# Performance work log

Measured on AMD Instinct MI355X. Metric: run time of the kernel, lower is better.

Reference implementation:

```python
import jax, jax.numpy as jnp
import numpy as np

EMBED_DIM = 512
NUM_HEADS = 8
HEAD_DIM = EMBED_DIM // NUM_HEADS
SEQ = 1024
BSZ = 8
T1 = 0.6
T2 = 0.4
MAX_NEG = -jnp.finfo(jnp.float32).max


def setup_inputs() -> dict:
    key = jax.random.key(0)
    ks = jax.random.split(key, 10)
    shp = (SEQ, BSZ, EMBED_DIM)
    inv = 1.0 / np.sqrt(EMBED_DIM)
    return {
        "query": jax.random.normal(ks[0], shp, jnp.float32),
        "key": jax.random.normal(ks[1], shp, jnp.float32),
        "value": jax.random.normal(ks[2], shp, jnp.float32),
        "query_sem": jax.random.normal(ks[3], shp, jnp.float32),
        "key_sem": jax.random.normal(ks[4], shp, jnp.float32),
        "sem_map": jax.random.uniform(ks[5], (SEQ, SEQ), jnp.float32),
        "in_proj_weight": jax.random.normal(ks[6], (3 * EMBED_DIM, EMBED_DIM), jnp.float32) * inv,
        "in_proj_bias": jnp.zeros((3 * EMBED_DIM,), jnp.float32),
        "out_proj_weight": jax.random.normal(ks[7], (EMBED_DIM, EMBED_DIM), jnp.float32) * inv,
        "out_proj_bias": jnp.zeros((EMBED_DIM,), jnp.float32),
    }


def _heads(x):
    # [T, B, E] -> [B*H, T, head_dim]
    T, B, E = x.shape
    return jnp.transpose(x.reshape(T, B * NUM_HEADS, HEAD_DIM), (1, 0, 2))


def _attn_path(qx, kx, vx, sem_map, Wi, bi, Wo, bo, ssa):
    # packed in-projection (generic path: q, k, v are distinct tensors)
    Wq, Wk, Wv = jnp.split(Wi, 3, axis=0)
    bq, bk, bv = jnp.split(bi, 3)
    q = _heads(qx @ Wq.T + bq)
    k = _heads(kx @ Wk.T + bk)
    v = _heads(vx @ Wv.T + bv)
    scale = 1.0 / np.sqrt(HEAD_DIM)
    scores = jnp.einsum("bte,bse->bts", q * scale, k)  # [B*H, T, S]
    scores = jnp.where(sem_map[None, :, :] < 0.5, MAX_NEG, scores)
    if ssa:
        # keep only the argmax entry per row, others set to max_neg
        idx = jnp.argmax(scores, axis=-1)  # [B*H, T]
        keep = jnp.arange(scores.shape[-1])[None, None, :] == idx[..., None]
        scores = jnp.where(keep, scores, MAX_NEG)
    w = jax.nn.softmax(scores, axis=-1)
    o = jnp.einsum("bts,bse->bte", w, v)  # [B*H, T, head_dim]
    o = jnp.transpose(o, (1, 0, 2)).reshape(SEQ, BSZ, EMBED_DIM)
    return o @ Wo.T + bo


def reference(query, key, value, query_sem, key_sem, sem_map, in_proj_weight, in_proj_bias, out_proj_weight, out_proj_bias):
    # SCA: semantic q/k attend, style value
    x_sca = _attn_path(query_sem, key_sem, value, sem_map, in_proj_weight, in_proj_bias, out_proj_weight, out_proj_bias, ssa=False)
    # SSA: content/style q/k, hard-argmax sparsified attention
    x_ssa = _attn_path(query, key, value, sem_map, in_proj_weight, in_proj_bias, out_proj_weight, out_proj_bias, ssa=True)
    return T1 * x_sca + T2 * x_ssa
```

## Files before the change

kernel.cpp:

```cpp
#include <hip/hip_runtime.h>
#include <float.h>


namespace {
constexpr int kSeq = 1024;
constexpr int kBsz = 8;
constexpr int kEmb = 512;
constexpr int kHD  = 64;
constexpr float kT1 = 0.6f;
constexpr float kT2 = 0.4f;
constexpr float kScale = 0.125f;
constexpr float kMargin = 0.125f;
constexpr int kCap = 256;
}

typedef short bf16x8 __attribute__((ext_vector_type(8)));
typedef float f32x4  __attribute__((ext_vector_type(4)));

union FragU { uint4 u4; bf16x8 f; uint u[4]; };

__device__ __forceinline__ ushort f2bf(float f) {
  uint u = __float_as_uint(f);
  u += 0x7fff + ((u >> 16) & 1);
  return (ushort)(u >> 16);
}
__device__ __forceinline__ uint pack2(float lo, float hi) {
  return (uint)f2bf(lo) | ((uint)f2bf(hi) << 16);
}
__device__ __forceinline__ float bf2f(uint h) {
  return __uint_as_float(h << 16);
}
__device__ __forceinline__ uint monokey(float v) {
  uint u = __float_as_uint(v);
  return (u & 0x80000000u) ? ~u : (u | 0x80000000u);
}
__device__ __forceinline__ uint combine2(uint m, uint s) {
  float lo = bf2f(m & 0xFFFF) + kT2 * bf2f(s & 0xFFFF);
  float hi = bf2f(m >> 16)    + kT2 * bf2f(s >> 16);
  return pack2(lo, hi);
}

__global__ void smask_prep(const float* __restrict__ SEM,
                           unsigned long long* __restrict__ SMASK) {
  const int t = blockIdx.x;
  const int w4 = threadIdx.x >> 6;
  const int lane = threadIdx.x & 63;
#pragma unroll
  for (int i = 0; i < 4; ++i) {
    const int word = (w4 << 2) + i;
    const float v = SEM[t * kSeq + (word << 6) + lane];
    unsigned long long m = __ballot(v >= 0.5f);
    if (lane == 0) SMASK[t * 16 + word] = m;
  }
}

__global__ __launch_bounds__(256, 4) void proj_ns(
    const float* __restrict__ Xq, const float* __restrict__ Xk,
    const float* __restrict__ W, const float* __restrict__ bias,
    float* __restrict__ OutQ, float* __restrict__ OutK)
{
  __shared__ float As[32 * 132];
  __shared__ float Bs[32 * 68];

  const int z = blockIdx.z;
  const float* X = z ? Xk : Xq;
  float* Out = z ? OutK : OutQ;
  const int woff = z << 9;

  const int mBase = blockIdx.x << 7;
  const int nBase = blockIdx.y << 6;
  const int tid = threadIdx.x;
  const int tx = tid & 15;
  const int my = tid >> 4;
  const int ar = tid >> 1, ah = (tid & 1) << 4;
  const int br = tid >> 2, bk = (tid & 3) << 3;

  float acc[8][4];
#pragma unroll
  for (int i = 0; i < 8; ++i)
#pragma unroll
    for (int j = 0; j < 4; ++j) acc[i][j] = 0.f;

  const float* xp = X + (size_t)(mBase + ar) * kEmb + ah;
  const float* wp = W + (size_t)(woff + nBase + br) * kEmb + bk;

  float4 a0 = ((const float4*)xp)[0];
  float4 a1 = ((const float4*)xp)[1];
  float4 a2 = ((const float4*)xp)[2];
  float4 a3 = ((const float4*)xp)[3];
  float4 b0 = ((const float4*)wp)[0];
  float4 b1 = ((const float4*)wp)[1];

  for (int k0 = 0; k0 < kEmb; k0 += 32) {
    __syncthreads();
    {
      float av[16] = {a0.x, a0.y, a0.z, a0.w, a1.x, a1.y, a1.z, a1.w,
                      a2.x, a2.y, a2.z, a2.w, a3.x, a3.y, a3.z, a3.w};
#pragma unroll
      for (int i = 0; i < 16; ++i) As[(ah + i) * 132 + ar] = av[i];
      float bv[8] = {b0.x, b0.y, b0.z, b0.w, b1.x, b1.y, b1.z, b1.w};
#pragma unroll
      for (int i = 0; i < 8; ++i) Bs[(bk + i) * 68 + br] = bv[i];
    }
    __syncthreads();

    const int kn = k0 + 32;
    if (kn < kEmb) {
      a0 = ((const float4*)(xp + kn))[0];
      a1 = ((const float4*)(xp + kn))[1];
      a2 = ((const float4*)(xp + kn))[2];
      a3 = ((const float4*)(xp + kn))[3];
      b0 = ((const float4*)(wp + kn))[0];
      b1 = ((const float4*)(wp + kn))[1];
    }

#pragma unroll 8
    for (int k = 0; k < 32; ++k) {
      float4 A0 = *(const float4*)&As[k * 132 + (my << 3)];
      float4 A1 = *(const float4*)&As[k * 132 + (my << 3) + 4];
      float4 Bv = *(const float4*)&Bs[k * 68 + (tx << 2)];
      float aa[8] = {A0.x, A0.y, A0.z, A0.w, A1.x, A1.y, A1.z, A1.w};
      float bb[4] = {Bv.x, Bv.y, Bv.z, Bv.w};
#pragma unroll
      for (int i = 0; i < 8; ++i)
#pragma unroll
        for (int j = 0; j < 4; ++j)
          acc[i][j] = fmaf(aa[i], bb[j], acc[i][j]);
    }
  }

#pragma unroll
  for (int i = 0; i < 8; ++i) {
    const int m = mBase + (my << 3) + i;
#pragma unroll
    for (int j = 0; j < 4; ++j) {
      const int n = nBase + (tx << 2) + j;
      const float v = acc[i][j] + bias[woff + n];
      const int oi = (((m & 7) << 3) + (n >> 6)) * (kSeq * kHD) +
                     ((m >> 3) << 6) + (n & 63);
      Out[oi] = v;
    }
  }
}

__global__ __launch_bounds__(256, 4) void gemm_sca(
    const float* __restrict__ X0, const float* __restrict__ X1,
    const float* __restrict__ X2,
    const float* __restrict__ W, const float* __restrict__ bias,
    ushort* __restrict__ Out16)
{
  __shared__ uint As[128 * 20];
  __shared__ uint Bs[64 * 20];

  const int z = blockIdx.z;
  const float* X = (z == 0) ? X0 : (z == 1) ? X1 : X2;
  const int woff = z << 9;
  const float scale = (z == 0) ? kScale : 1.0f;
  const size_t zoff = (size_t)z * ((size_t)kSeq * kBsz * kEmb);

  const int mBase = blockIdx.x << 7;
  const int nBase = blockIdx.y << 6;
  const int tid = threadIdx.x;
  const int w = tid >> 6;
  const int l = tid & 63;
  const int l15 = l & 15;
  const int quad = l >> 4;
  const int wm = w & 1, wn = w >> 1;

  const int srow = tid >> 1;
  const int shalf = tid & 1;

  f32x4 acc[4][2];
#pragma unroll
  for (int mi = 0; mi < 4; ++mi)
#pragma unroll
    for (int ni = 0; ni < 2; ++ni) acc[mi][ni] = (f32x4){0.f, 0.f, 0.f, 0.f};

  float4 ra0, ra1, ra2, ra3;
  float4 rb0, rb1, rb2, rb3;

#define GLOADF(kk) do {                                                    \
    const float* xp_ = X + (size_t)(mBase + srow) * kEmb + (kk) +          \
                       (shalf << 4);                                       \
    ra0 = ((const float4*)xp_)[0];                                         \
    ra1 = ((const float4*)xp_)[1];                                         \
    ra2 = ((const float4*)xp_)[2];                                         \
    ra3 = ((const float4*)xp_)[3];                                         \
    if (tid < 128) {                                                       \
      const float* wp_ = W + (size_t)(woff + nBase + srow) * kEmb + (kk) + \
                         (shalf << 4);                                     \
      rb0 = ((const float4*)wp_)[0];                                       \
      rb1 = ((const float4*)wp_)[1];                                       \
      rb2 = ((const float4*)wp_)[2];                                       \
      rb3 = ((const float4*)wp_)[3];                                       \
    }                                                                      \
  } while (0)

  GLOADF(0);

  for (int k0 = 0; k0 < kEmb; k0 += 32) {
    uint4 ah0, ah1, bw0, bw1;
    ah0 = make_uint4(pack2(ra0.x, ra0.y), pack2(ra0.z, ra0.w),
                     pack2(ra1.x, ra1.y), pack2(ra1.z, ra1.w));
    ah1 = make_uint4(pack2(ra2.x, ra2.y), pack2(ra2.z, ra2.w),
                     pack2(ra3.x, ra3.y), pack2(ra3.z, ra3.w));
    if (tid < 128) {
      bw0 = make_uint4(pack2(rb0.x, rb0.y), pack2(rb0.z, rb0.w),
                       pack2(rb1.x, rb1.y), pack2(rb1.z, rb1.w));
      bw1 = make_uint4(pack2(rb2.x, rb2.y), pack2(rb2.z, rb2.w),
                       pack2(rb3.x, rb3.y), pack2(rb3.z, rb3.w));
    }
    __syncthreads();
    {
      uint* dst = As + srow * 20 + (shalf << 3);
      ((uint4*)dst)[0] = ah0;
      ((uint4*)dst)[1] = ah1;
      if (tid < 128) {
        uint* db = Bs + srow * 20 + (shalf << 3);
        ((uint4*)db)[0] = bw0;
        ((uint4*)db)[1] = bw1;
      }
    }
    __syncthreads();

    if (k0 + 32 < kEmb) GLOADF(k0 + 32);

    FragU aF[4], bF[2];
#pragma unroll
    for (int ni = 0; ni < 2; ++ni)
      bF[ni].u4 = *(const uint4*)(Bs + ((wn << 5) + (ni << 4) + l15) * 20 + (quad << 2));
#pragma unroll
    for (int mi = 0; mi < 4; ++mi)
      aF[mi].u4 = *(const uint4*)(As + ((wm << 6) + (mi << 4) + l15) * 20 + (quad << 2));
#pragma unroll
    for (int mi = 0; mi < 4; ++mi)
#pragma unroll
      for (int ni = 0; ni < 2; ++ni)
        acc[mi][ni] = __builtin_amdgcn_mfma_f32_16x16x32_bf16(
            aF[mi].f, bF[ni].f, acc[mi][ni], 0, 0, 0);
  }
#undef GLOADF

#pragma unroll
  for (int ni = 0; ni < 2; ++ni) {
    const int n = nBase + (wn << 5) + (ni << 4) + l15;
    const float bv = bias[woff + n];
#pragma unroll
    for (int mi = 0; mi < 4; ++mi) {
#pragma unroll
      for (int r = 0; r < 4; ++r) {
        const int m = mBase + (wm << 6) + (mi << 4) + (quad << 2) + r;
        const float v = acc[mi][ni][r] + bv;
        const int oi = (((m & 7) << 3) + (n >> 6)) * (kSeq * kHD) +
                       ((m >> 3) << 6) + (n & 63);
        Out16[zoff + oi] = f2bf(v * scale);
      }
    }
  }
}

__device__ __forceinline__ void sca_body(
    uint* ks, uint* vt, uint* ps, int idx, int bh,
    const ushort* __restrict__ Q16, const ushort* __restrict__ K16,
    const ushort* __restrict__ V16,
    const unsigned long long* __restrict__ SMASK,
    ushort* __restrict__ MIX16)
{
  const int t0  = idx << 6;
  const int tid = threadIdx.x;
  const int w    = tid >> 6;
  const int l    = tid & 63;
  const int l15  = l & 15;
  const int quad = l >> 4;

  const uint* Qu = (const uint*)Q16 + (size_t)bh * (kSeq * 32);
  const uint* Ku = (const uint*)K16 + (size_t)bh * (kSeq * 32);
  const uint* Vu = (const uint*)V16 + (size_t)bh * (kSeq * 32);

  FragU qf0, qf1;
  {
    const uint* qrow = Qu + (size_t)(t0 + (w << 4) + l15) * 32;
    qf0.u4 = *(const uint4*)(qrow + (quad << 2));
    qf1.u4 = *(const uint4*)(qrow + 16 + (quad << 2));
  }

  f32x4 oacc[4];
#pragma unroll
  for (int nt = 0; nt < 4; ++nt) oacc[nt] = (f32x4){0.f, 0.f, 0.f, 0.f};
  float den[4] = {0.f, 0.f, 0.f, 0.f};

  uint* psw = ps + w * 576;

  const int sl = tid >> 2, c = tid & 3;
  const int p = tid >> 3, c7 = tid & 7;

  uint4 pk0 = ((const uint4*)(Ku + (size_t)sl * 32 + (c << 3)))[0];
  uint4 pk1 = ((const uint4*)(Ku + (size_t)sl * 32 + (c << 3)))[1];
  uint4 pv0 = *(const uint4*)(Vu + (size_t)(p << 1) * 32 + (c7 << 2));
  uint4 pv1 = *(const uint4*)(Vu + (size_t)(p << 1) * 32 + (c7 << 2) + 32);

  for (int s0 = 0, tile = 0; s0 < kSeq; s0 += 64, ++tile) {
    __syncthreads();
    {
      uint* dst = ks + sl * 36 + (c << 3);
      ((uint4*)dst)[0] = pk0;
      ((uint4*)dst)[1] = pk1;
    }
    {
      FragU A, B;
      A.u4 = pv0;
      B.u4 = pv1;
      const int Wp = (p + ((c7 & 3) << 2)) & 31;
#pragma unroll
      for (int i = 0; i < 8; ++i) {
        uint ai = (A.u[i >> 1] >> ((i & 1) << 4)) & 0xFFFF;
        uint bi = (B.u[i >> 1] >> ((i & 1) << 4)) & 0xFFFF;
        vt[((c7 << 3) + i) * 36 + Wp] = ai | (bi << 16);
      }
    }
    __syncthreads();

    if (s0 + 64 < kSeq) {
      const uint* kp = Ku + (size_t)(s0 + 64 + sl) * 32 + (c << 3);
      pk0 = ((const uint4*)kp)[0];
      pk1 = ((const uint4*)kp)[1];
      const uint* va = Vu + (size_t)(s0 + 64 + (p << 1)) * 32 + (c7 << 2);
      pv0 = *(const uint4*)va;
      pv1 = *(const uint4*)(va + 32);
    }

    unsigned long long wv[4];
#pragma unroll
    for (int r = 0; r < 4; ++r)
      wv[r] = SMASK[(size_t)(t0 + (w << 4) + (quad << 2) + r) * 16 + tile];

#pragma unroll
    for (int st = 0; st < 4; ++st) {
      f32x4 sacc = (f32x4){0.f, 0.f, 0.f, 0.f};
      const int srow = (st << 4) + l15;
      FragU kf0, kf1;
      kf0.u4 = *(const uint4*)(ks + srow * 36 + (quad << 2));
      kf1.u4 = *(const uint4*)(ks + srow * 36 + 16 + (quad << 2));
      sacc = __builtin_amdgcn_mfma_f32_16x16x32_bf16(qf0.f, kf0.f, sacc, 0, 0, 0);
      sacc = __builtin_amdgcn_mfma_f32_16x16x32_bf16(qf1.f, kf1.f, sacc, 0, 0, 0);

#pragma unroll
      for (int r = 0; r < 4; ++r) {
        const int trow = (quad << 2) + r;
        const uint bit = (uint)(wv[r] >> ((st << 4) + l15)) & 1u;
        const float val = bit ? __expf(sacc[r]) : 0.f;
        den[r] += val;
        const int W  = (st << 3) + (l15 >> 1);
        const int Wp = (W + (((trow >> 3) & 1) << 3)) & 31;
        ushort* p16 = (ushort*)(psw + trow * 36 + Wp);
        p16[l15 & 1] = f2bf(val);
      }
    }
#pragma unroll
    for (int ch = 0; ch < 2; ++ch) {
      FragU pf;
      const int pw = ((ch << 4) + (quad << 2) + (((l15 >> 3) & 1) << 3)) & 31;
      pf.u4 = *(const uint4*)(psw + l15 * 36 + pw);
#pragma unroll
      for (int nt = 0; nt < 4; ++nt) {
        const int d = (nt << 4) + l15;
        const int vw = ((ch << 4) + (quad << 2) + (((d >> 3) & 3) << 2)) & 31;
        FragU vf;
        vf.u4 = *(const uint4*)(vt + d * 36 + vw);
        oacc[nt] = __builtin_amdgcn_mfma_f32_16x16x32_bf16(pf.f, vf.f, oacc[nt], 0, 0, 0);
      }
    }
  }

#pragma unroll
  for (int r = 0; r < 4; ++r) {
    float d = den[r];
    d += __shfl_xor(d, 1);
    d += __shfl_xor(d, 2);
    d += __shfl_xor(d, 4);
    d += __shfl_xor(d, 8);
    den[r] = kT1 / d;
  }
  const int b = bh >> 3, h = bh & 7;
#pragma unroll
  for (int nt = 0; nt < 4; ++nt) {
#pragma unroll
    for (int r = 0; r < 4; ++r) {
      const int t = t0 + (w << 4) + (quad << 2) + r;
      const int d = (nt << 4) + l15;
      MIX16[(size_t)(t * kBsz + b) * kEmb + (h << 6) + d] =
          f2bf(oacc[nt][r] * den[r]);
    }
  }
}

__device__ __forceinline__ void ssa_body(
    uint* ks, uint2* list2, float* thrL, unsigned long long* key64,
    uint* cnt, int idx, int bh,
    const float* __restrict__ Qf, const float* __restrict__ Kf,
    const ushort* __restrict__ V16,
    const unsigned long long* __restrict__ SMASK,
    ushort* __restrict__ SSAV16)
{
  const int t0  = idx << 6;
  const int tid = threadIdx.x;
  const int w    = tid >> 6;
  const int l    = tid & 63;
  const int l15  = l & 15;
  const int quad = l >> 4;

  if (tid < 4) cnt[tid] = 0;
  if (tid < 64) key64[tid] = 0ull;

  const float* Qh = Qf + (size_t)bh * (kSeq * kHD);
  const float* Kh = Kf + (size_t)bh * (kSeq * kHD);

  FragU qf0, qf1;
  {
    const float* qrow = Qh + (size_t)(t0 + (w << 4) + l15) * kHD;
    float4 q0 = *(const float4*)(qrow + (quad << 3));
    float4 q1 = *(const float4*)(qrow + (quad << 3) + 4);
    float4 q2 = *(const float4*)(qrow + 32 + (quad << 3));
    float4 q3 = *(const float4*)(qrow + 32 + (quad << 3) + 4);
    qf0.u4 = make_uint4(pack2(q0.x * kScale, q0.y * kScale),
                        pack2(q0.z * kScale, q0.w * kScale),
                        pack2(q1.x * kScale, q1.y * kScale),
                        pack2(q1.z * kScale, q1.w * kScale));
    qf1.u4 = make_uint4(pack2(q2.x * kScale, q2.y * kScale),
                        pack2(q2.z * kScale, q2.w * kScale),
                        pack2(q3.x * kScale, q3.y * kScale),
                        pack2(q3.z * kScale, q3.w * kScale));
  }

  float m4[4] = {-FLT_MAX, -FLT_MAX, -FLT_MAX, -FLT_MAX};

  const int sl = tid >> 2, c4 = tid & 3;
  const float* kp = Kh + (size_t)sl * kHD + (c4 << 4);
  float4 pk0 = ((const float4*)kp)[0];
  float4 pk1 = ((const float4*)kp)[1];
  float4 pk2 = ((const float4*)kp)[2];
  float4 pk3 = ((const float4*)kp)[3];

  for (int s0 = 0, tile = 0; s0 < kSeq; s0 += 64, ++tile) {
    __syncthreads();
    {
      uint4 w0 = make_uint4(pack2(pk0.x, pk0.y), pack2(pk0.z, pk0.w),
                            pack2(pk1.x, pk1.y), pack2(pk1.z, pk1.w));
      uint4 w1 = make_uint4(pack2(pk2.x, pk2.y), pack2(pk2.z, pk2.w),
                            pack2(pk3.x, pk3.y), pack2(pk3.z, pk3.w));
      uint* dst = ks + sl * 36 + (c4 << 3);
      ((uint4*)dst)[0] = w0;
      ((uint4*)dst)[1] = w1;
    }
    __syncthreads();

    if (s0 + 64 < kSeq) {
      const float* kn = Kh + (size_t)(s0 + 64 + sl) * kHD + (c4 << 4);
      pk0 = ((const float4*)kn)[0];
      pk1 = ((const float4*)kn)[1];
      pk2 = ((const float4*)kn)[2];
      pk3 = ((const float4*)kn)[3];
    }

    unsigned long long wv[4];
#pragma unroll
    for (int r = 0; r < 4; ++r)
      wv[r] = SMASK[(size_t)(t0 + (w << 4) + (quad << 2) + r) * 16 + tile];

    f32x4 sv[4];
#pragma unroll
    for (int st = 0; st < 4; ++st) {
      f32x4 sacc = (f32x4){0.f, 0.f, 0.f, 0.f};
      const int srow = (st << 4) + l15;
      FragU kf0, kf1;
      kf0.u4 = *(const uint4*)(ks + srow * 36 + (quad << 2));
      kf1.u4 = *(const uint4*)(ks + srow * 36 + 16 + (quad << 2));
      sacc = __builtin_amdgcn_mfma_f32_16x16x32_bf16(qf0.f, kf0.f, sacc, 0, 0, 0);
      sacc = __builtin_amdgcn_mfma_f32_16x16x32_bf16(qf1.f, kf1.f, sacc, 0, 0, 0);
      sv[st] = sacc;
#pragma unroll
      for (int r = 0; r < 4; ++r) {
        const uint bit = (uint)(wv[r] >> ((st << 4) + l15)) & 1u;
        if (bit) m4[r] = fmaxf(m4[r], sacc[r]);
      }
    }
#pragma unroll
    for (int r = 0; r < 4; ++r) {
      float m = m4[r];
      m = fmaxf(m, __shfl_xor(m, 1));
      m = fmaxf(m, __shfl_xor(m, 2));
      m = fmaxf(m, __shfl_xor(m, 4));
      m = fmaxf(m, __shfl_xor(m, 8));
      m4[r] = m;
    }
#pragma unroll
    for (int st = 0; st < 4; ++st) {
#pragma unroll
      for (int r = 0; r < 4; ++r) {
        const uint bit = (uint)(wv[r] >> ((st << 4) + l15)) & 1u;
        const float x = sv[st][r];
        if (bit && x >= m4[r] - kMargin) {
          uint idx2 = atomicAdd(&cnt[w], 1u);
          if (idx2 < (uint)kCap) {
            const int rowid = (quad << 2) + r;
            const int s = s0 + (st << 4) + l15;
            list2[w * kCap + idx2] = make_uint2(__float_as_uint(x),
                                                ((uint)rowid << 10) | (uint)s);
          }
        }
      }
    }
  }

  if (l15 == 0) {
#pragma unroll
    for (int r = 0; r < 4; ++r) thrL[w * 16 + (quad << 2) + r] = m4[r] - kMargin;
  }
  __syncthreads();

  const uint n = min(cnt[w], (uint)kCap);
  for (uint base = 0; base < n; base += 64) {
    const uint e = base + (uint)l;
    if (e < n) {
      const uint2 ent = list2[w * kCap + e];
      const uint rowid = ent.y >> 10;
      const uint s = ent.y & 1023u;
      const float xv = __uint_as_float(ent.x);
      if (xv >= thrL[w * 16 + rowid]) {
        const int t = t0 + (w << 4) + (int)rowid;
        const float* qe = Qh + (size_t)t * kHD;
        const float* ke = Kh + (size_t)s * kHD;
        float p0 = 0.f, p1 = 0.f, p2 = 0.f, p3 = 0.f;
#pragma unroll
        for (int i = 0; i < 16; ++i) {
          float4 qq = *(const float4*)(qe + (i << 2));
          float4 kk = *(const float4*)(ke + (i << 2));
          p0 = fmaf(qq.x, kk.x, p0);
          p1 = fmaf(qq.y, kk.y, p1);
          p2 = fmaf(qq.z, kk.z, p2);
          p3 = fmaf(qq.w, kk.w, p3);
        }
        const float acc = ((p0 + p1) + (p2 + p3)) * kScale;
        const unsigned long long key =
            ((unsigned long long)monokey(acc) << 16) |
            (unsigned long long)(1023u - s);
        atomicMax(&key64[w * 16 + rowid], key);
      }
    }
  }
  __syncthreads();

  const int b = bh >> 3, h = bh & 7;
  const uint* Vu = (const uint*)V16 + (size_t)bh * (kSeq * 32);
#pragma unroll
  for (int r = 0; r < 4; ++r) {
    const int rowid = (quad << 2) + r;
    const unsigned long long key = key64[w * 16 + rowid];
    const uint s = 1023u - (uint)(key & 0xFFFFull);
    const uint2 vv = *(const uint2*)(Vu + (size_t)s * 32 + (l15 << 1));
    const int t = t0 + (w << 4) + rowid;
    uint* op = (uint*)SSAV16 + ((size_t)(t * kBsz + b) * kEmb + (h << 6)) / 2 + (l15 << 1);
    *(uint2*)op = vv;
  }
}

__global__ __launch_bounds__(256, 4) void back_fused(
    const ushort* __restrict__ Q16, const ushort* __restrict__ K16,
    const ushort* __restrict__ V16,
    const float* __restrict__ P0, const float* __restrict__ P1,
    const unsigned long long* __restrict__ SMASK,
    ushort* __restrict__ MIX16, ushort* __restrict__ SSAV16)
{
  __shared__ unsigned long long lds8[3456];
  uint* base = (uint*)lds8;

  const int role = blockIdx.x & 1;
  const int idx  = blockIdx.x >> 1;
  const int bh   = blockIdx.y;

  if (role == 0) {
    sca_body(base, base + 2304, base + 4608, idx, bh,
             Q16, K16, V16, SMASK, MIX16);
  } else {
    ssa_body(base, (uint2*)(base + 2304), (float*)(base + 4352),
             (unsigned long long*)(base + 4416), base + 4544,
             idx, bh, P0, P1, V16, SMASK, SSAV16);
  }
}

__global__ __launch_bounds__(256, 4) void gemm_out(
    const ushort* __restrict__ MIX16, const ushort* __restrict__ SSAV16,
    const float* __restrict__ W, const float* __restrict__ bias,
    float* __restrict__ OutF)
{
  __shared__ uint As[128 * 20];
  __shared__ uint Bs[64 * 20];

  const int mBase = blockIdx.x << 7;
  const int nBase = blockIdx.y << 6;
  const int tid = threadIdx.x;
  const int w = tid >> 6;
  const int l = tid & 63;
  const int l15 = l & 15;
  const int quad = l >> 4;
  const int wm = w & 1, wn = w >> 1;

  const int srow = tid >> 1;
  const int shalf = tid & 1;

  f32x4 acc[4][2];
#pragma unroll
  for (int mi = 0; mi < 4; ++mi)
#pragma unroll
    for (int ni = 0; ni < 2; ++ni) acc[mi][ni] = (f32x4){0.f, 0.f, 0.f, 0.f};

  uint4 qa0, qa1, qb0, qb1;
  float4 rb0, rb1, rb2, rb3;

#define GLOADO(kk) do {                                                    \
    const size_t off_ = (size_t)(mBase + srow) * 256 + ((kk) >> 1) +       \
                        (shalf << 3);                                      \
    const uint* ma_ = (const uint*)MIX16 + off_;                           \
    qa0 = ((const uint4*)ma_)[0];                                          \
    qa1 = ((const uint4*)ma_)[1];                                          \
    const uint* sa_ = (const uint*)SSAV16 + off_;                          \
    qb0 = ((const uint4*)sa_)[0];                                          \
    qb1 = ((const uint4*)sa_)[1];                                          \
    if (tid < 128) {                                                       \
      const float* wp_ = W + (size_t)(nBase + srow) * kEmb + (kk) +        \
                         (shalf << 4);                                     \
      rb0 = ((const float4*)wp_)[0];                                       \
      rb1 = ((const float4*)wp_)[1];                                       \
      rb2 = ((const float4*)wp_)[2];                                       \
      rb3 = ((const float4*)wp_)[3];                                       \
    }                                                                      \
  } while (0)

  GLOADO(0);

  for (int k0 = 0; k0 < kEmb; k0 += 32) {
    uint4 ah0, ah1, bw0, bw1;
    ah0 = make_uint4(combine2(qa0.x, qb0.x), combine2(qa0.y, qb0.y),
                     combine2(qa0.z, qb0.z), combine2(qa0.w, qb0.w));
    ah1 = make_uint4(combine2(qa1.x, qb1.x), combine2(qa1.y, qb1.y),
                     combine2(qa1.z, qb1.z), combine2(qa1.w, qb1.w));
    if (tid < 128) {
      bw0 = make_uint4(pack2(rb0.x, rb0.y), pack2(rb0.z, rb0.w),
                       pack2(rb1.x, rb1.y), pack2(rb1.z, rb1.w));
      bw1 = make_uint4(pack2(rb2.x, rb2.y), pack2(rb2.z, rb2.w),
                       pack2(rb3.x, rb3.y), pack2(rb3.z, rb3.w));
    }
    __syncthreads();
    {
      uint* dst = As + srow * 20 + (shalf << 3);
      ((uint4*)dst)[0] = ah0;
      ((uint4*)dst)[1] = ah1;
      if (tid < 128) {
        uint* db = Bs + srow * 20 + (shalf << 3);
        ((uint4*)db)[0] = bw0;
        ((uint4*)db)[1] = bw1;
      }
    }
    __syncthreads();

    if (k0 + 32 < kEmb) GLOADO(k0 + 32);

    FragU aF[4], bF[2];
#pragma unroll
    for (int ni = 0; ni < 2; ++ni)
      bF[ni].u4 = *(const uint4*)(Bs + ((wn << 5) + (ni << 4) + l15) * 20 + (quad << 2));
#pragma unroll
    for (int mi = 0; mi < 4; ++mi)
      aF[mi].u4 = *(const uint4*)(As + ((wm << 6) + (mi << 4) + l15) * 20 + (quad << 2));
#pragma unroll
    for (int mi = 0; mi < 4; ++mi)
#pragma unroll
      for (int ni = 0; ni < 2; ++ni)
        acc[mi][ni] = __builtin_amdgcn_mfma_f32_16x16x32_bf16(
            aF[mi].f, bF[ni].f, acc[mi][ni], 0, 0, 0);
  }
#undef GLOADO

#pragma unroll
  for (int ni = 0; ni < 2; ++ni) {
    const int n = nBase + (wn << 5) + (ni << 4) + l15;
    const float bv = bias[n];
#pragma unroll
    for (int mi = 0; mi < 4; ++mi) {
#pragma unroll
      for (int r = 0; r < 4; ++r) {
        const int m = mBase + (wm << 6) + (mi << 4) + (quad << 2) + r;
        const float v = acc[mi][ni][r] + bv;
        OutF[(size_t)m * kEmb + n] = v;
      }
    }
  }
}

extern "C" void kernel_launch(void* const* d_in, const int* in_sizes, int n_in,
                              void* d_out, int out_size, void* d_ws, size_t ws_size,
                              hipStream_t stream) {
  const float* query  = (const float*)d_in[0];
  const float* key    = (const float*)d_in[1];
  const float* value  = (const float*)d_in[2];
  const float* qsem   = (const float*)d_in[3];
  const float* ksem   = (const float*)d_in[4];
  const float* semmap = (const float*)d_in[5];
  const float* Wi     = (const float*)d_in[6];
  const float* bi     = (const float*)d_in[7];
  const float* Wo     = (const float*)d_in[8];
  const float* bo     = (const float*)d_in[9];
  float* out = (float*)d_out;

  char* ws = (char*)d_ws;
  unsigned long long* SMASK = (unsigned long long*)ws;           ws += 1024 * 16 * 8;
  ushort* Q16   = (ushort*)ws; ws += (size_t)64 * kSeq * kHD * 2;
  ushort* K16   = (ushort*)ws; ws += (size_t)64 * kSeq * kHD * 2;
  ushort* V16   = (ushort*)ws; ws += (size_t)64 * kSeq * kHD * 2;
  ushort* MIX16 = (ushort*)ws; ws += (size_t)kSeq * kBsz * kEmb * 2;
  ushort* SSAV16= (ushort*)ws; ws += (size_t)kSeq * kBsz * kEmb * 2;
  float* P1 = (float*)ws;      ws += (size_t)64 * kSeq * kHD * 4;
  float* P0 = out;

  const dim3 gp(64, 8, 2);
  const dim3 g3(64, 8, 3);

  smask_prep<<<1024, 256, 0, stream>>>(semmap, SMASK);
  gemm_sca<<<g3, 256, 0, stream>>>(qsem, ksem, value, Wi, bi, Q16);
  proj_ns<<<gp, 256, 0, stream>>>(query, key, Wi, bi, P0, P1);
  back_fused<<<dim3(32, 64), 256, 0, stream>>>(Q16, K16, V16, P0, P1,
                                               SMASK, MIX16, SSAV16);
  gemm_out<<<dim3(64, 8), 256, 0, stream>>>(MIX16, SSAV16, Wo, bo, out);
}
```

Before: 425.9 us.

## Prepack inputs to bf16, split fused attention kernel, merge SSA output into MIX buffer

Adds a prepack kernel that converts the semantic/value inputs and both weight matrices to bf16 once. The input and output projection GEMMs then load bf16 directly instead of converting fp32 in their inner loops. The role-split back_fused kernel is replaced by separate SCA and SSA kernels, with SSA now using 512 threads and 128-row tiles. SSA adds its 0.4-weighted contribution into MIX16 in place, which removes the SSAV16 buffer and the combine step in the output GEMM. In exchange there is an extra full pass over the inputs, the SCA/SSA overlap is lost, and the SSA read-modify-write on MIX16 depends on kernel ordering.

Result: faster. 401.3 us (-5.8%).

```diff
diff --git a/kernel.cpp b/kernel.cpp
--- a/kernel.cpp
+++ b/kernel.cpp
@@ -34,10 +34,31 @@
   uint u = __float_as_uint(v);
   return (u & 0x80000000u) ? ~u : (u | 0x80000000u);
 }
-__device__ __forceinline__ uint combine2(uint m, uint s) {
-  float lo = bf2f(m & 0xFFFF) + kT2 * bf2f(s & 0xFFFF);
-  float hi = bf2f(m >> 16)    + kT2 * bf2f(s >> 16);
-  return pack2(lo, hi);
+
+__global__ __launch_bounds__(256, 8) void prepack(
+    const float* __restrict__ X0, const float* __restrict__ X1,
+    const float* __restrict__ X2, const float* __restrict__ Wif,
+    const float* __restrict__ Wof,
+    ushort* __restrict__ X16, ushort* __restrict__ Wi16,
+    ushort* __restrict__ Wo16)
+{
+  const int z = blockIdx.y;
+  const float* src;
+  ushort* dst;
+  size_t count;
+  if (z == 0)      { src = X0;  dst = X16;                count = 4194304; }
+  else if (z == 1) { src = X1;  dst = X16 + 4194304;      count = 4194304; }
+  else if (z == 2) { src = X2;  dst = X16 + 2 * 4194304;  count = 4194304; }
+  else if (z == 3) { src = Wif; dst = Wi16;               count = 786432; }
+  else             { src = Wof; dst = Wo16;               count = 262144; }
+
+  const size_t idx = ((size_t)blockIdx.x * 256 + threadIdx.x) * 8;
+  if (idx >= count) return;
+  float4 f0 = *(const float4*)(src + idx);
+  float4 f1 = *(const float4*)(src + idx + 4);
+  uint4 o = make_uint4(pack2(f0.x, f0.y), pack2(f0.z, f0.w),
+                       pack2(f1.x, f1.y), pack2(f1.z, f1.w));
+  *(uint4*)(dst + idx) = o;
 }
 
 __global__ void smask_prep(const float* __restrict__ SEM,
@@ -143,20 +164,19 @@
   }
 }
 
-__global__ __launch_bounds__(256, 4) void gemm_sca(
-    const float* __restrict__ X0, const float* __restrict__ X1,
-    const float* __restrict__ X2,
-    const float* __restrict__ W, const float* __restrict__ bias,
-    ushort* __restrict__ Out16)
+__global__ __launch_bounds__(256, 4) void gemm_sca16(
+    const ushort* __restrict__ X16, const ushort* __restrict__ Wi16,
+    const float* __restrict__ bias, ushort* __restrict__ Out16)
 {
   __shared__ uint As[128 * 20];
   __shared__ uint Bs[64 * 20];
 
   const int z = blockIdx.z;
-  const float* X = (z == 0) ? X0 : (z == 1) ? X1 : X2;
   const int woff = z << 9;
   const float scale = (z == 0) ? kScale : 1.0f;
   const size_t zoff = (size_t)z * ((size_t)kSeq * kBsz * kEmb);
+  const uint* Xu = (const uint*)X16 + (size_t)z * (8192 * 256);
+  const uint* Wu = (const uint*)Wi16;
 
   const int mBase = blockIdx.x << 7;
   const int nBase = blockIdx.y << 6;
@@ -176,40 +196,25 @@
 #pragma unroll
     for (int ni = 0; ni < 2; ++ni) acc[mi][ni] = (f32x4){0.f, 0.f, 0.f, 0.f};
 
-  float4 ra0, ra1, ra2, ra3;
-  float4 rb0, rb1, rb2, rb3;
-
-#define GLOADF(kk) do {                                                    \
-    const float* xp_ = X + (size_t)(mBase + srow) * kEmb + (kk) +          \
-                       (shalf << 4);                                       \
-    ra0 = ((const float4*)xp_)[0];                                         \
-    ra1 = ((const float4*)xp_)[1];                                         \
-    ra2 = ((const float4*)xp_)[2];                                         \
-    ra3 = ((const float4*)xp_)[3];                                         \
+  uint4 qa0, qa1, qb0, qb1;
+
+#define GLOAD16(kk) do {                                                   \
+    const uint* xs_ = Xu + (size_t)(mBase + srow) * 256 + ((kk) >> 1) +    \
+                      (shalf << 3);                                        \
+    qa0 = ((const uint4*)xs_)[0];                                          \
+    qa1 = ((const uint4*)xs_)[1];                                          \
     if (tid < 128) {                                                       \
-      const float* wp_ = W + (size_t)(woff + nBase + srow) * kEmb + (kk) + \
-                         (shalf << 4);                                     \
-      rb0 = ((const float4*)wp_)[0];                                       \
-      rb1 = ((const float4*)wp_)[1];                                       \
-      rb2 = ((const float4*)wp_)[2];                                       \
-      rb3 = ((const float4*)wp_)[3];                                       \
+      const uint* ws_ = Wu + (size_t)(woff + nBase + srow) * 256 +         \
+                        ((kk) >> 1) + (shalf << 3);                        \
+      qb0 = ((const uint4*)ws_)[0];                                        \
+      qb1 = ((const uint4*)ws_)[1];                                        \
     }                                                                      \
   } while (0)
 
-  GLOADF(0);
+  GLOAD16(0);
 
   for (int k0 = 0; k0 < kEmb; k0 += 32) {
-    uint4 ah0, ah1, bw0, bw1;
-    ah0 = make_uint4(pack2(ra0.x, ra0.y), pack2(ra0.z, ra0.w),
-                     pack2(ra1.x, ra1.y), pack2(ra1.z, ra1.w));
-    ah1 = make_uint4(pack2(ra2.x, ra2.y), pack2(ra2.z, ra2.w),
-                     pack2(ra3.x, ra3.y), pack2(ra3.z, ra3.w));
-    if (tid < 128) {
-      bw0 = make_uint4(pack2(rb0.x, rb0.y), pack2(rb0.z, rb0.w),
-                       pack2(rb1.x, rb1.y), pack2(rb1.z, rb1.w));
-      bw1 = make_uint4(pack2(rb2.x, rb2.y), pack2(rb2.z, rb2.w),
-                       pack2(rb3.x, rb3.y), pack2(rb3.z, rb3.w));
-    }
+    uint4 ah0 = qa0, ah1 = qa1, bw0 = qb0, bw1 = qb1;
     __syncthreads();
     {
       uint* dst = As + srow * 20 + (shalf << 3);
@@ -223,7 +228,7 @@
     }
     __syncthreads();
 
-    if (k0 + 32 < kEmb) GLOADF(k0 + 32);
+    if (k0 + 32 < kEmb) GLOAD16(k0 + 32);
 
     FragU aF[4], bF[2];
 #pragma unroll
@@ -239,7 +244,7 @@
         acc[mi][ni] = __builtin_amdgcn_mfma_f32_16x16x32_bf16(
             aF[mi].f, bF[ni].f, acc[mi][ni], 0, 0, 0);
   }
-#undef GLOADF
+#undef GLOAD16
 
 #pragma unroll
   for (int ni = 0; ni < 2; ++ni) {
@@ -259,14 +264,18 @@
   }
 }
 
-__device__ __forceinline__ void sca_body(
-    uint* ks, uint* vt, uint* ps, int idx, int bh,
+__global__ __launch_bounds__(256, 4) void sca_mfma2(
     const ushort* __restrict__ Q16, const ushort* __restrict__ K16,
     const ushort* __restrict__ V16,
     const unsigned long long* __restrict__ SMASK,
     ushort* __restrict__ MIX16)
 {
-  const int t0  = idx << 6;
+  __shared__ uint ks[64 * 36];
+  __shared__ uint vt[64 * 36];
+  __shared__ uint ps[4][16 * 36];
+
+  const int t0  = blockIdx.x << 6;
+  const int bh  = blockIdx.y;
   const int tid = threadIdx.x;
   const int w    = tid >> 6;
   const int l    = tid & 63;
@@ -289,7 +298,7 @@
   for (int nt = 0; nt < 4; ++nt) oacc[nt] = (f32x4){0.f, 0.f, 0.f, 0.f};
   float den[4] = {0.f, 0.f, 0.f, 0.f};
 
-  uint* psw = ps + w * 576;
+  uint* psw = ps[w];
 
   const int sl = tid >> 2, c = tid & 3;
   const int p = tid >> 3, c7 = tid & 7;
@@ -394,23 +403,28 @@
   }
 }
 
-__device__ __forceinline__ void ssa_body(
-    uint* ks, uint2* list2, float* thrL, unsigned long long* key64,
-    uint* cnt, int idx, int bh,
+__global__ __launch_bounds__(512, 4) void ssa_v3f(
     const float* __restrict__ Qf, const float* __restrict__ Kf,
     const ushort* __restrict__ V16,
     const unsigned long long* __restrict__ SMASK,
-    ushort* __restrict__ SSAV16)
+    ushort* __restrict__ MIX16)
 {
-  const int t0  = idx << 6;
+  __shared__ uint ks[64 * 36];
+  __shared__ uint2 list[8][kCap];
+  __shared__ float thrL[8][16];
+  __shared__ unsigned long long key64L[8][16];
+  __shared__ uint cnt[8];
+
+  const int t0  = blockIdx.x << 7;
+  const int bh  = blockIdx.y;
   const int tid = threadIdx.x;
   const int w    = tid >> 6;
   const int l    = tid & 63;
   const int l15  = l & 15;
   const int quad = l >> 4;
 
-  if (tid < 4) cnt[tid] = 0;
-  if (tid < 64) key64[tid] = 0ull;
+  if (tid < 8) cnt[tid] = 0;
+  if (tid < 128) ((unsigned long long*)key64L)[tid] = 0ull;
 
   const float* Qh = Qf + (size_t)bh * (kSeq * kHD);
   const float* Kh = Kf + (size_t)bh * (kSeq * kHD);
@@ -434,32 +448,24 @@
 
   float m4[4] = {-FLT_MAX, -FLT_MAX, -FLT_MAX, -FLT_MAX};
 
-  const int sl = tid >> 2, c4 = tid & 3;
-  const float* kp = Kh + (size_t)sl * kHD + (c4 << 4);
-  float4 pk0 = ((const float4*)kp)[0];
-  float4 pk1 = ((const float4*)kp)[1];
-  float4 pk2 = ((const float4*)kp)[2];
-  float4 pk3 = ((const float4*)kp)[3];
+  const int krow = tid >> 3, kc = tid & 7;
+  const float* kp0 = Kh + (size_t)krow * kHD + (kc << 3);
+  float4 pkf0 = ((const float4*)kp0)[0];
+  float4 pkf1 = ((const float4*)kp0)[1];
 
   for (int s0 = 0, tile = 0; s0 < kSeq; s0 += 64, ++tile) {
     __syncthreads();
     {
-      uint4 w0 = make_uint4(pack2(pk0.x, pk0.y), pack2(pk0.z, pk0.w),
-                            pack2(pk1.x, pk1.y), pack2(pk1.z, pk1.w));
-      uint4 w1 = make_uint4(pack2(pk2.x, pk2.y), pack2(pk2.z, pk2.w),
-                            pack2(pk3.x, pk3.y), pack2(pk3.z, pk3.w));
-      uint* dst = ks + sl * 36 + (c4 << 3);
-      ((uint4*)dst)[0] = w0;
-      ((uint4*)dst)[1] = w1;
+      uint4 w0 = make_uint4(pack2(pkf0.x, pkf0.y), pack2(pkf0.z, pkf0.w),
+                            pack2(pkf1.x, pkf1.y), pack2(pkf1.z, pkf1.w));
+      *(uint4*)(ks + krow * 36 + (kc << 2)) = w0;
     }
     __syncthreads();
 
     if (s0 + 64 < kSeq) {
-      const float* kn = Kh + (size_t)(s0 + 64 + sl) * kHD + (c4 << 4);
-      pk0 = ((const float4*)kn)[0];
-      pk1 = ((const float4*)kn)[1];
-      pk2 = ((const float4*)kn)[2];
-      pk3 = ((const float4*)kn)[3];
+      const float* kn = Kh + (size_t)(s0 + 64 + krow) * kHD + (kc << 3);
+      pkf0 = ((const float4*)kn)[0];
+      pkf1 = ((const float4*)kn)[1];
     }
 
     unsigned long long wv[4];
@@ -500,12 +506,12 @@
         const uint bit = (uint)(wv[r] >> ((st << 4) + l15)) & 1u;
         const float x = sv[st][r];
         if (bit && x >= m4[r] - kMargin) {
-          uint idx2 = atomicAdd(&cnt[w], 1u);
-          if (idx2 < (uint)kCap) {
+          uint idx = atomicAdd(&cnt[w], 1u);
+          if (idx < (uint)kCap) {
             const int rowid = (quad << 2) + r;
             const int s = s0 + (st << 4) + l15;
-            list2[w * kCap + idx2] = make_uint2(__float_as_uint(x),
-                                                ((uint)rowid << 10) | (uint)s);
+            list[w][idx] = make_uint2(__float_as_uint(x),
+                                      ((uint)rowid << 10) | (uint)s);
           }
         }
       }
@@ -514,7 +520,7 @@
 
   if (l15 == 0) {
 #pragma unroll
-    for (int r = 0; r < 4; ++r) thrL[w * 16 + (quad << 2) + r] = m4[r] - kMargin;
+    for (int r = 0; r < 4; ++r) thrL[w][(quad << 2) + r] = m4[r] - kMargin;
   }
   __syncthreads();
 
@@ -522,11 +528,11 @@
   for (uint base = 0; base < n; base += 64) {
     const uint e = base + (uint)l;
     if (e < n) {
-      const uint2 ent = list2[w * kCap + e];
+      const uint2 ent = list[w][e];
       const uint rowid = ent.y >> 10;
       const uint s = ent.y & 1023u;
       const float xv = __uint_as_float(ent.x);
-      if (xv >= thrL[w * 16 + rowid]) {
+      if (xv >= thrL[w][rowid]) {
         const int t = t0 + (w << 4) + (int)rowid;
         const float* qe = Qh + (size_t)t * kHD;
         const float* ke = Kh + (size_t)s * kHD;
@@ -544,7 +550,7 @@
         const unsigned long long key =
             ((unsigned long long)monokey(acc) << 16) |
             (unsigned long long)(1023u - s);
-        atomicMax(&key64[w * 16 + rowid], key);
+        atomicMax(&key64L[w][rowid], key);
       }
     }
   }
@@ -555,43 +561,23 @@
 #pragma unroll
   for (int r = 0; r < 4; ++r) {
     const int rowid = (quad << 2) + r;
-    const unsigned long long key = key64[w * 16 + rowid];
+    const unsigned long long key = key64L[w][rowid];
     const uint s = 1023u - (uint)(key & 0xFFFFull);
     const uint2 vv = *(const uint2*)(Vu + (size_t)s * 32 + (l15 << 1));
     const int t = t0 + (w << 4) + rowid;
-    uint* op = (uint*)SSAV16 + ((size_t)(t * kBsz + b) * kEmb + (h << 6)) / 2 + (l15 << 1);
-    *(uint2*)op = vv;
-  }
-}
-
-__global__ __launch_bounds__(256, 4) void back_fused(
-    const ushort* __restrict__ Q16, const ushort* __restrict__ K16,
-    const ushort* __restrict__ V16,
-    const float* __restrict__ P0, const float* __restrict__ P1,
-    const unsigned long long* __restrict__ SMASK,
-    ushort* __restrict__ MIX16, ushort* __restrict__ SSAV16)
-{
-  __shared__ unsigned long long lds8[3456];
-  uint* base = (uint*)lds8;
-
-  const int role = blockIdx.x & 1;
-  const int idx  = blockIdx.x >> 1;
-  const int bh   = blockIdx.y;
-
-  if (role == 0) {
-    sca_body(base, base + 2304, base + 4608, idx, bh,
-             Q16, K16, V16, SMASK, MIX16);
-  } else {
-    ssa_body(base, (uint2*)(base + 2304), (float*)(base + 4352),
-             (unsigned long long*)(base + 4416), base + 4544,
-             idx, bh, P0, P1, V16, SMASK, SSAV16);
-  }
-}
-
-__global__ __launch_bounds__(256, 4) void gemm_out(
-    const ushort* __restrict__ MIX16, const ushort* __restrict__ SSAV16,
-    const float* __restrict__ W, const float* __restrict__ bias,
-    float* __restrict__ OutF)
+    uint* op = (uint*)MIX16 + ((size_t)(t * kBsz + b) * kEmb + (h << 6)) / 2 + (l15 << 1);
+    uint2 o = *(uint2*)op;
+    float o0 = bf2f(o.x & 0xFFFF) + kT2 * bf2f(vv.x & 0xFFFF);
+    float o1 = bf2f(o.x >> 16)    + kT2 * bf2f(vv.x >> 16);
+    float o2 = bf2f(o.y & 0xFFFF) + kT2 * bf2f(vv.y & 0xFFFF);
+    float o3 = bf2f(o.y >> 16)    + kT2 * bf2f(vv.y >> 16);
+    *(uint2*)op = make_uint2(pack2(o0, o1), pack2(o2, o3));
+  }
+}
+
+__global__ __launch_bounds__(256, 4) void gemm_out16(
+    const ushort* __restrict__ MIX16, const ushort* __restrict__ Wo16,
+    const float* __restrict__ bias, float* __restrict__ OutF)
 {
   __shared__ uint As[128 * 20];
   __shared__ uint Bs[64 * 20];
@@ -615,41 +601,24 @@
     for (int ni = 0; ni < 2; ++ni) acc[mi][ni] = (f32x4){0.f, 0.f, 0.f, 0.f};
 
   uint4 qa0, qa1, qb0, qb1;
-  float4 rb0, rb1, rb2, rb3;
 
 #define GLOADO(kk) do {                                                    \
-    const size_t off_ = (size_t)(mBase + srow) * 256 + ((kk) >> 1) +       \
-                        (shalf << 3);                                      \
-    const uint* ma_ = (const uint*)MIX16 + off_;                           \
+    const uint* ma_ = (const uint*)MIX16 + (size_t)(mBase + srow) * 256 +  \
+                      ((kk) >> 1) + (shalf << 3);                          \
     qa0 = ((const uint4*)ma_)[0];                                          \
     qa1 = ((const uint4*)ma_)[1];                                          \
-    const uint* sa_ = (const uint*)SSAV16 + off_;                          \
-    qb0 = ((const uint4*)sa_)[0];                                          \
-    qb1 = ((const uint4*)sa_)[1];                                          \
     if (tid < 128) {                                                       \
-      const float* wp_ = W + (size_t)(nBase + srow) * kEmb + (kk) +        \
-                         (shalf << 4);                                     \
-      rb0 = ((const float4*)wp_)[0];                                       \
-      rb1 = ((const float4*)wp_)[1];                                       \
-      rb2 = ((const float4*)wp_)[2];                                       \
-      rb3 = ((const float4*)wp_)[3];                                       \
+      const uint* ws_ = (const uint*)Wo16 + (size_t)(nBase + srow) * 256 + \
+                        ((kk) >> 1) + (shalf << 3);                        \
+      qb0 = ((const uint4*)ws_)[0];                                        \
+      qb1 = ((const uint4*)ws_)[1];                                        \
     }                                                                      \
   } while (0)
 
   GLOADO(0);
 
   for (int k0 = 0; k0 < kEmb; k0 += 32) {
-    uint4 ah0, ah1, bw0, bw1;
-    ah0 = make_uint4(combine2(qa0.x, qb0.x), combine2(qa0.y, qb0.y),
-                     combine2(qa0.z, qb0.z), combine2(qa0.w, qb0.w));
-    ah1 = make_uint4(combine2(qa1.x, qb1.x), combine2(qa1.y, qb1.y),
-                     combine2(qa1.z, qb1.z), combine2(qa1.w, qb1.w));
-    if (tid < 128) {
-      bw0 = make_uint4(pack2(rb0.x, rb0.y), pack2(rb0.z, rb0.w),
-                       pack2(rb1.x, rb1.y), pack2(rb1.z, rb1.w));
-      bw1 = make_uint4(pack2(rb2.x, rb2.y), pack2(rb2.z, rb2.w),
-                       pack2(rb3.x, rb3.y), pack2(rb3.z, rb3.w));
-    }
+    uint4 ah0 = qa0, ah1 = qa1, bw0 = qb0, bw1 = qb1;
     __syncthreads();
     {
       uint* dst = As + srow * 20 + (shalf << 3);
@@ -718,17 +687,25 @@
   ushort* K16   = (ushort*)ws; ws += (size_t)64 * kSeq * kHD * 2;
   ushort* V16   = (ushort*)ws; ws += (size_t)64 * kSeq * kHD * 2;
   ushort* MIX16 = (ushort*)ws; ws += (size_t)kSeq * kBsz * kEmb * 2;
-  ushort* SSAV16= (ushort*)ws; ws += (size_t)kSeq * kBsz * kEmb * 2;
-  float* P1 = (float*)ws;      ws += (size_t)64 * kSeq * kHD * 4;
+  ushort* Wi16  = (ushort*)ws; ws += (size_t)3 * kEmb * kEmb * 2;
+  ushort* Wo16  = (ushort*)ws; ws += (size_t)kEmb * kEmb * 2;
+  ushort* X16 = (ushort*)ws;
+  float*  P1  = (float*)ws;    ws += (size_t)3 * kSeq * kBsz * kEmb * 2;
   float* P0 = out;
 
+  const dim3 gpk(2048, 5);
   const dim3 gp(64, 8, 2);
   const dim3 g3(64, 8, 3);
-
+  const dim3 go(64, 8);
+  const dim3 gs(16, 64);
+  const dim3 gv(8, 64);
+
+  prepack<<<gpk, 256, 0, stream>>>(qsem, ksem, value, Wi, Wo,
+                                   X16, Wi16, Wo16);
   smask_prep<<<1024, 256, 0, stream>>>(semmap, SMASK);
-  gemm_sca<<<g3, 256, 0, stream>>>(qsem, ksem, value, Wi, bi, Q16);
+  gemm_sca16<<<g3, 256, 0, stream>>>(X16, Wi16, bi, Q16);
   proj_ns<<<gp, 256, 0, stream>>>(query, key, Wi, bi, P0, P1);
-  back_fused<<<dim3(32, 64), 256, 0, stream>>>(Q16, K16, V16, P0, P1,
-                                               SMASK, MIX16, SSAV16);
-  gemm_out<<<dim3(64, 8), 256, 0, stream>>>(MIX16, SSAV16, Wo, bo, out);
-}
+  sca_mfma2<<<gs, 64 * 4, 0, stream>>>(Q16, K16, V16, SMASK, MIX16);
+  ssa_v3f<<<gv, 512, 0, stream>>>(P0, P1, V16, SMASK, MIX16);
+  gemm_out16<<<go, 256, 0, stream>>>(MIX16, Wo16, bo, out);
+}
```
